# Performance work log

Measured on AMD Instinct MI355X. Metric: run time of the kernel, lower is better.

## Reference

```python
import jax, jax.numpy as jnp
import numpy as np

BATCH = 128
N = 4096
STEPNUM = 100
X = 10.0
DX = X / N               # grid spacing
BETA = 0.1
DT = 0.75 * DX / 1.5     # CFL-stable dt per module's update() rule (max|f'| ~ 1.5)


def _flux(u):
    # f_real with is_real=True:
    # f = 0.5*u*(3 - u^2) + beta/12 * u^2 * (3/4 - 2u + 3/2 u^2 - 1/4 u^4)
    u2 = u * u
    return 0.5 * u * (3.0 - u2) + (BETA / 12.0) * u2 * (0.75 - 2.0 * u + 1.5 * u2 - 0.25 * u2 * u2)


def _dflux(u):
    # analytic df/du (same value torch.autograd.grad computes in df_du)
    u2 = u * u
    u3 = u2 * u
    return 1.5 - 1.5 * u2 + (BETA / 12.0) * (1.5 * u - 6.0 * u2 + 6.0 * u3 - 1.5 * u2 * u3)


def setup_inputs() -> dict:
    key = jax.random.key(0)
    init = jax.random.uniform(key, (BATCH, N), dtype=jnp.float32)  # [B, N] in [0,1)
    return {"init": init, "stepnum": STEPNUM}


def reference(init, stepnum):
    r = jnp.float32(DT / DX)

    def step(u, _):
        f = _flux(u)                       # [B, N]
        a = jnp.abs(_dflux(u))             # [B, N], |f'(u)|
        # local Lax-Friedrichs speed: max over each adjacent pair (== torch.max over 2-slice)
        amax = jnp.maximum(a[:, :-1], a[:, 1:])                     # [B, N-1]
        f_half = 0.5 * (f[:, :-1] + f[:, 1:]) - 0.5 * amax * (u[:, 1:] - u[:, :-1])
        interior = u[:, 1:-1] - r * (f_half[:, 1:] - f_half[:, :-1])  # [B, N-2]
        # boundary copy: u[:,0]=u[:,1], u[:,N-1]=u[:,N-2]
        u_new = jnp.concatenate([interior[:, :1], interior, interior[:, -1:]], axis=1)
        return u_new, u_new

    _, traj = jax.lax.scan(step, init, None, length=stepnum - 1)  # [stepnum-1, B, N]
    return jnp.concatenate([init[None], traj], axis=0)           # [stepnum, B, N]
```

## Files before the change

kernel.cpp:

```cpp
#include <hip/hip_runtime.h>

#define BATCH 128
#define NPTS  4096
#define HALF  2048
#define TPB   576
#define EPT   4
#define CWID  (TPB * EPT)
#define HALO  (CWID - HALF)

__device__ __forceinline__ void flux_eval(float u, float& g, float& ah) {
    constexpr float b  = 0.1f / 12.0f;
    constexpr float c6 = 0.5f * (-0.25f * b);
    constexpr float c4 = 0.5f * ( 1.5f  * b);
    constexpr float c3 = 0.5f * (-0.5f - 2.0f * b);
    constexpr float c2 = 0.5f * ( 0.75f * b);
    constexpr float c1 = 0.5f * ( 1.5f);
    constexpr float d5 = 0.5f * (-1.5f * b);
    constexpr float d3 = 0.5f * ( 6.0f * b);
    constexpr float d2 = 0.5f * (-(1.5f + 6.0f * b));
    constexpr float d1 = 0.5f * ( 1.5f * b);
    constexpr float d0 = 0.5f * ( 1.5f);

    float t = c6 * u;
    t = fmaf(t, u, c4);
    t = fmaf(t, u, c3);
    t = fmaf(t, u, c2);
    t = fmaf(t, u, c1);
    g = u * t;

    float e = d5 * u;
    e = fmaf(e, u, d3);
    e = fmaf(e, u, d2);
    e = fmaf(e, u, d1);
    e = fmaf(e, u, d0);
    ah = fabsf(e);
}

__global__ __launch_bounds__(TPB) void pde_rows_split(
        const float* __restrict__ init,
        const int*   __restrict__ stepnum_p,
        float*       __restrict__ out) {
    __shared__ __align__(8) float2 edge[2][TPB];

    const int blk  = blockIdx.x;
    const int row  = blk >> 1;
    const int half = blk & 1;
    const int tid  = threadIdx.x;
    const int base = half ? (NPTS - CWID) : 0;
    const int g0   = base + (tid << 2);
    const int stepnum = *stepnum_p;

    const bool ownstore = half ? (tid >= (HALO >> 2)) : (tid < (HALF >> 2));
    const bool rowL = (half == 0) && (tid == 0);
    const bool rowR = (half == 1) && (tid == TPB - 1);
    const int  tl = (tid == 0) ? 0 : tid - 1;
    const int  tr = (tid == TPB - 1) ? tid : tid + 1;

    float4 v4 = *(const float4*)(init + (size_t)row * NPTS + g0);
    float v0 = v4.x, v1 = v4.y, v2 = v4.z, v3 = v4.w;

    if (ownstore)
        *(float4*)(out + (size_t)row * NPTS + g0) = v4;

    int buf = 0;
    for (int s = 1; s < stepnum; ++s) {
        edge[buf][tid] = make_float2(v0, v3);
        asm volatile("s_waitcnt lgkmcnt(0)\n\ts_barrier" ::: "memory");
        const float vl = edge[buf][tl].y;
        const float vr = edge[buf][tr].x;
        buf ^= 1;

        float g[6], a[6];
        flux_eval(vl, g[0], a[0]);
        flux_eval(v0, g[1], a[1]);
        flux_eval(v1, g[2], a[2]);
        flux_eval(v2, g[3], a[3]);
        flux_eval(v3, g[4], a[4]);
        flux_eval(vr, g[5], a[5]);

        const float vv[6] = { vl, v0, v1, v2, v3, vr };
        float fh[5];
#pragma unroll
        for (int m = 0; m < 5; ++m)
            fh[m] = g[m] + g[m + 1] - fmaxf(a[m], a[m + 1]) * (vv[m + 1] - vv[m]);

        float u0 = fmaf(-0.5f, fh[1] - fh[0], v0);
        float u1 = fmaf(-0.5f, fh[2] - fh[1], v1);
        float u2 = fmaf(-0.5f, fh[3] - fh[2], v2);
        float u3 = fmaf(-0.5f, fh[4] - fh[3], v3);
        if (rowL) u0 = u1;
        if (rowR) u3 = u2;
        v0 = u0; v1 = u1; v2 = u2; v3 = u3;

        if (ownstore)
            *(float4*)(out + (size_t)s * ((size_t)BATCH * NPTS)
                           + (size_t)row * NPTS + g0)
                = make_float4(v0, v1, v2, v3);
    }
}

extern "C" void kernel_launch(void* const* d_in, const int* in_sizes, int n_in,
                              void* d_out, int out_size, void* d_ws, size_t ws_size,
                              hipStream_t stream) {
    const float* init  = (const float*)d_in[0];
    const int*   steps = (const int*)d_in[1];
    float*       out   = (float*)d_out;
    pde_rows_split<<<BATCH * 2, TPB, 0, stream>>>(init, steps, out);
}
```

Measured before the change: 215.9 us.

## Replace block-split rows with independent wavefronts using redundant halo computation

Each row is split into 14 overlapping segments, one 64-lane wavefront each. Every segment has a 104-point halo on each side, wide enough to absorb all steps without any inter-wave exchange. Neighbour values move through wave shuffles instead of LDS plus a block barrier, and each lane now handles 8 points. The cost is substantial redundant flux computation in the halos, traded for removing per-step synchronisation.

```diff
diff --git a/kernel.cpp b/kernel.cpp
--- a/kernel.cpp
+++ b/kernel.cpp
@@ -2,11 +2,12 @@
 
 #define BATCH 128
 #define NPTS  4096
-#define HALF  2048
-#define TPB   576
-#define EPT   4
-#define CWID  (TPB * EPT)
-#define HALO  (CWID - HALF)
+#define EPT   8
+#define WREG  (64 * EPT)
+#define HALOC 104
+#define OWN   (WREG - 2 * HALOC)
+#define SEGS  14
+#define TPB   64
 
 __device__ __forceinline__ void flux_eval(float u, float& g, float& ah) {
     constexpr float b  = 0.1f / 12.0f;
@@ -36,66 +37,67 @@
     ah = fabsf(e);
 }
 
-__global__ __launch_bounds__(TPB) void pde_rows_split(
+__global__ __launch_bounds__(TPB) void pde_wave_indep(
         const float* __restrict__ init,
         const int*   __restrict__ stepnum_p,
         float*       __restrict__ out) {
-    __shared__ __align__(8) float2 edge[2][TPB];
+    const int wid  = blockIdx.x;
+    const int lane = threadIdx.x;
+    const int row  = wid / SEGS;
+    const int seg  = wid - row * SEGS;
 
-    const int blk  = blockIdx.x;
-    const int row  = blk >> 1;
-    const int half = blk & 1;
-    const int tid  = threadIdx.x;
-    const int base = half ? (NPTS - CWID) : 0;
-    const int g0   = base + (tid << 2);
+    const int ownlo = seg * OWN;
+    const int base  = min(max(ownlo - HALOC, 0), NPTS - WREG);
+    const int c0    = base + lane * EPT;
+    const bool ownstore = (c0 >= ownlo) && (c0 < ownlo + OWN) && (c0 < NPTS);
+    const bool bcL = (seg == 0) && (lane == 0);
+    const bool bcR = (seg == SEGS - 1) && (lane == 63);
     const int stepnum = *stepnum_p;
 
-    const bool ownstore = half ? (tid >= (HALO >> 2)) : (tid < (HALF >> 2));
-    const bool rowL = (half == 0) && (tid == 0);
-    const bool rowR = (half == 1) && (tid == TPB - 1);
-    const int  tl = (tid == 0) ? 0 : tid - 1;
-    const int  tr = (tid == TPB - 1) ? tid : tid + 1;
+    const float* ip = init + (size_t)row * NPTS + c0;
+    const float4 A  = *(const float4*)ip;
+    const float4 Bv = *(const float4*)(ip + 4);
+    float v[EPT] = {A.x, A.y, A.z, A.w, Bv.x, Bv.y, Bv.z, Bv.w};
 
-    float4 v4 = *(const float4*)(init + (size_t)row * NPTS + g0);
-    float v0 = v4.x, v1 = v4.y, v2 = v4.z, v3 = v4.w;
+    float* op = out + (size_t)row * NPTS + c0;
+    const size_t zstride = (size_t)BATCH * NPTS;
 
-    if (ownstore)
-        *(float4*)(out + (size_t)row * NPTS + g0) = v4;
+    if (ownstore) {
+        *(float4*)op       = A;
+        *(float4*)(op + 4) = Bv;
+    }
 
-    int buf = 0;
     for (int s = 1; s < stepnum; ++s) {
-        edge[buf][tid] = make_float2(v0, v3);
-        asm volatile("s_waitcnt lgkmcnt(0)\n\ts_barrier" ::: "memory");
-        const float vl = edge[buf][tl].y;
-        const float vr = edge[buf][tr].x;
-        buf ^= 1;
+        const float vl = __shfl_up(v[EPT - 1], 1, 64);
+        const float vr = __shfl_down(v[0], 1, 64);
 
-        float g[6], a[6];
-        flux_eval(vl, g[0], a[0]);
-        flux_eval(v0, g[1], a[1]);
-        flux_eval(v1, g[2], a[2]);
-        flux_eval(v2, g[3], a[3]);
-        flux_eval(v3, g[4], a[4]);
-        flux_eval(vr, g[5], a[5]);
+        float vv[EPT + 2];
+        vv[0] = vl;
+#pragma unroll
+        for (int i = 0; i < EPT; ++i) vv[i + 1] = v[i];
+        vv[EPT + 1] = vr;
 
-        const float vv[6] = { vl, v0, v1, v2, v3, vr };
-        float fh[5];
+        float g[EPT + 2], a[EPT + 2];
 #pragma unroll
-        for (int m = 0; m < 5; ++m)
+        for (int i = 0; i < EPT + 2; ++i) flux_eval(vv[i], g[i], a[i]);
+
+        float fh[EPT + 1];
+#pragma unroll
+        for (int m = 0; m < EPT + 1; ++m)
             fh[m] = g[m] + g[m + 1] - fmaxf(a[m], a[m + 1]) * (vv[m + 1] - vv[m]);
 
-        float u0 = fmaf(-0.5f, fh[1] - fh[0], v0);
-        float u1 = fmaf(-0.5f, fh[2] - fh[1], v1);
-        float u2 = fmaf(-0.5f, fh[3] - fh[2], v2);
-        float u3 = fmaf(-0.5f, fh[4] - fh[3], v3);
-        if (rowL) u0 = u1;
-        if (rowR) u3 = u2;
-        v0 = u0; v1 = u1; v2 = u2; v3 = u3;
+#pragma unroll
+        for (int i = 0; i < EPT; ++i)
+            v[i] = fmaf(-0.5f, fh[i + 1] - fh[i], v[i]);
 
-        if (ownstore)
-            *(float4*)(out + (size_t)s * ((size_t)BATCH * NPTS)
-                           + (size_t)row * NPTS + g0)
-                = make_float4(v0, v1, v2, v3);
+        if (bcL) v[0] = v[1];
+        if (bcR) v[EPT - 1] = v[EPT - 2];
+
+        op += zstride;
+        if (ownstore) {
+            *(float4*)op       = make_float4(v[0], v[1], v[2], v[3]);
+            *(float4*)(op + 4) = make_float4(v[4], v[5], v[6], v[7]);
+        }
     }
 }
 
@@ -105,5 +107,5 @@
     const float* init  = (const float*)d_in[0];
     const int*   steps = (const int*)d_in[1];
     float*       out   = (float*)d_out;
-    pde_rows_split<<<BATCH * 2, TPB, 0, stream>>>(init, steps, out);
+    pde_wave_indep<<<BATCH * SEGS, TPB, 0, stream>>>(init, steps, out);
 }
```

Result: slower. 222.8 us (+3.2%).

## Stage output timesteps in LDS and flush them in bursts of eight

Applied to the files above, without the earlier changes.

Each step's owned results now go into a shared-memory plane buffer instead of straight to global memory. After every eight steps, the first 512 threads copy all staged planes out to global. This decouples global stores from the per-step barrier loop so that one burst of stores can overlap. The cost is 64KB of LDS per block, which may lower occupancy, plus two extra barriers per burst and an idle compute phase while the burst drains.

```diff
diff --git a/kernel.cpp b/kernel.cpp
--- a/kernel.cpp
+++ b/kernel.cpp
@@ -7,6 +7,9 @@
 #define EPT   4
 #define CWID  (TPB * EPT)
 #define HALO  (CWID - HALF)
+#define KPL   8
+
+typedef float v4f __attribute__((ext_vector_type(4)));
 
 __device__ __forceinline__ void flux_eval(float u, float& g, float& ah) {
     constexpr float b  = 0.1f / 12.0f;
@@ -36,11 +39,12 @@
     ah = fabsf(e);
 }
 
-__global__ __launch_bounds__(TPB) void pde_rows_split(
+__global__ __launch_bounds__(TPB) void pde_lds_burst(
         const float* __restrict__ init,
         const int*   __restrict__ stepnum_p,
         float*       __restrict__ out) {
-    __shared__ __align__(8) float2 edge[2][TPB];
+    __shared__ __align__(16) float planes[KPL][HALF];
+    __shared__ __align__(8)  float2 edge[2][TPB];
 
     const int blk  = blockIdx.x;
     const int row  = blk >> 1;
@@ -51,51 +55,73 @@
     const int stepnum = *stepnum_p;
 
     const bool ownstore = half ? (tid >= (HALO >> 2)) : (tid < (HALF >> 2));
+    const int  ownidx   = half ? (g0 - HALF) : g0;
     const bool rowL = (half == 0) && (tid == 0);
     const bool rowR = (half == 1) && (tid == TPB - 1);
     const int  tl = (tid == 0) ? 0 : tid - 1;
     const int  tr = (tid == TPB - 1) ? tid : tid + 1;
 
-    float4 v4 = *(const float4*)(init + (size_t)row * NPTS + g0);
+    const float4 v4 = *(const float4*)(init + (size_t)row * NPTS + g0);
     float v0 = v4.x, v1 = v4.y, v2 = v4.z, v3 = v4.w;
 
     if (ownstore)
         *(float4*)(out + (size_t)row * NPTS + g0) = v4;
 
+    const size_t Z = (size_t)BATCH * NPTS;
+    const int ownbase = half ? HALF : 0;
+
     int buf = 0;
-    for (int s = 1; s < stepnum; ++s) {
-        edge[buf][tid] = make_float2(v0, v3);
+    int s = 1;
+    while (s < stepnum) {
+        const int K = min(KPL, stepnum - s);
+        for (int k = 0; k < K; ++k) {
+            edge[buf][tid] = make_float2(v0, v3);
+            asm volatile("s_waitcnt lgkmcnt(0)\n\ts_barrier" ::: "memory");
+            const float vl = edge[buf][tl].y;
+            const float vr = edge[buf][tr].x;
+            buf ^= 1;
+
+            float g[6], a[6];
+            flux_eval(vl, g[0], a[0]);
+            flux_eval(v0, g[1], a[1]);
+            flux_eval(v1, g[2], a[2]);
+            flux_eval(v2, g[3], a[3]);
+            flux_eval(v3, g[4], a[4]);
+            flux_eval(vr, g[5], a[5]);
+
+            const float vv[6] = { vl, v0, v1, v2, v3, vr };
+            float fh[5];
+#pragma unroll
+            for (int m = 0; m < 5; ++m)
+                fh[m] = g[m] + g[m + 1] - fmaxf(a[m], a[m + 1]) * (vv[m + 1] - vv[m]);
+
+            float u0 = fmaf(-0.5f, fh[1] - fh[0], v0);
+            float u1 = fmaf(-0.5f, fh[2] - fh[1], v1);
+            float u2 = fmaf(-0.5f, fh[3] - fh[2], v2);
+            float u3 = fmaf(-0.5f, fh[4] - fh[3], v3);
+            if (rowL) u0 = u1;
+            if (rowR) u3 = u2;
+            v0 = u0; v1 = u1; v2 = u2; v3 = u3;
+
+            if (ownstore)
+                *(v4f*)&planes[k][ownidx] = (v4f){v0, v1, v2, v3};
+        }
+
         asm volatile("s_waitcnt lgkmcnt(0)\n\ts_barrier" ::: "memory");
-        const float vl = edge[buf][tl].y;
-        const float vr = edge[buf][tr].x;
-        buf ^= 1;
 
-        float g[6], a[6];
-        flux_eval(vl, g[0], a[0]);
-        flux_eval(v0, g[1], a[1]);
-        flux_eval(v1, g[2], a[2]);
-        flux_eval(v2, g[3], a[3]);
-        flux_eval(v3, g[4], a[4]);
-        flux_eval(vr, g[5], a[5]);
+        if (tid < (HALF >> 2)) {
+            float* dst = out + (size_t)s * Z + (size_t)row * NPTS + ownbase + (tid << 2);
+#pragma unroll
+            for (int p = 0; p < KPL; ++p) {
+                if (p < K) {
+                    const v4f t = *(const v4f*)&planes[p][tid << 2];
+                    *(v4f*)(dst + (size_t)p * Z) = t;
+                }
+            }
+        }
 
-        const float vv[6] = { vl, v0, v1, v2, v3, vr };
-        float fh[5];
-#pragma unroll
-        for (int m = 0; m < 5; ++m)
-            fh[m] = g[m] + g[m + 1] - fmaxf(a[m], a[m + 1]) * (vv[m + 1] - vv[m]);
-
-        float u0 = fmaf(-0.5f, fh[1] - fh[0], v0);
-        float u1 = fmaf(-0.5f, fh[2] - fh[1], v1);
-        float u2 = fmaf(-0.5f, fh[3] - fh[2], v2);
-        float u3 = fmaf(-0.5f, fh[4] - fh[3], v3);
-        if (rowL) u0 = u1;
-        if (rowR) u3 = u2;
-        v0 = u0; v1 = u1; v2 = u2; v3 = u3;
-
-        if (ownstore)
-            *(float4*)(out + (size_t)s * ((size_t)BATCH * NPTS)
-                           + (size_t)row * NPTS + g0)
-                = make_float4(v0, v1, v2, v3);
+        asm volatile("s_waitcnt lgkmcnt(0)\n\ts_barrier" ::: "memory");
+        s += K;
     }
 }
 
@@ -105,5 +131,5 @@
     const float* init  = (const float*)d_in[0];
     const int*   steps = (const int*)d_in[1];
     float*       out   = (float*)d_out;
-    pde_rows_split<<<BATCH * 2, TPB, 0, stream>>>(init, steps, out);
+    pde_lds_burst<<<BATCH * 2, TPB, 0, stream>>>(init, steps, out);
 }
```

After: 226.6 us. +4.9%, slower.
